# Optimization experiments

Hardware: AMD Instinct MI355X
Metric: run time of the kernel (lower is better)

Reference implementation:

```python
import jax, jax.numpy as jnp
import numpy as np

N_NODES = 100000
N_EDGES = 1_600_000
D_EMB = 64
D_HID = 128


def setup_inputs() -> dict:
    key = jax.random.key(0)
    k1, k2, k3, k4 = jax.random.split(key, 4)
    emb = jax.random.normal(k1, (N_NODES, D_EMB), dtype=jnp.float32)
    W1 = jax.random.normal(k2, (D_EMB, D_HID), dtype=jnp.float32) * 0.05
    b1 = jnp.zeros((D_HID,), dtype=jnp.float32)
    W2 = jax.random.normal(k3, (D_HID, D_EMB), dtype=jnp.float32) * 0.05
    b2 = jnp.zeros((D_EMB,), dtype=jnp.float32)
    edge_index = jax.random.randint(k4, (2, N_EDGES), 0, N_NODES, dtype=jnp.int64 if jax.config.jax_enable_x64 else jnp.int32)
    return {"emb": emb, "W1": W1, "b1": b1, "W2": W2, "b2": b2,
            "edge_index": edge_index, "num_nodes": N_NODES}


def _gcn_conv(x, W, b, src, dst, deg_inv_sqrt, num_nodes):
    # PyG GCNConv: linear transform, then normalized scatter-add aggregation.
    x = x @ W                                   # [N, out]
    norm = deg_inv_sqrt[src] * deg_inv_sqrt[dst]  # [E+N]
    msg = x[src] * norm[:, None]                # gather + scale
    out = jax.ops.segment_sum(msg, dst, num_segments=num_nodes)
    return out + b


def reference(emb, W1, b1, W2, b2, edge_index, num_nodes):
    # Add self-loops (PyG GCNConv default add_self_loops=True).
    loops = jnp.arange(num_nodes, dtype=edge_index.dtype)
    src = jnp.concatenate([edge_index[0], loops])
    dst = jnp.concatenate([edge_index[1], loops])
    # Symmetric normalization degree (computed on destination, incl. loops).
    deg = jax.ops.segment_sum(jnp.ones(src.shape, dtype=emb.dtype), dst,
                              num_segments=num_nodes)
    dinv = jnp.where(deg > 0, jax.lax.rsqrt(jnp.maximum(deg, 1e-12)), 0.0)

    x = _gcn_conv(emb, W1, b1, src, dst, dinv, num_nodes)
    x = jax.nn.relu(x)
    x = _gcn_conv(x, W2, b2, src, dst, dinv, num_nodes)
    return x
```

## Files before the change

### kernel.cpp

```cpp
#include <hip/hip_runtime.h>


constexpr int D_EMB = 64;
constexpr int D_HID = 128;
constexpr int CB_LOG = 9;
constexpr int CB = 1 << CB_LOG;
constexpr int CAP = 16384;
constexpr int FB_EPT = 16;
constexpr int FB_CHUNK = 256 * FB_EPT;

__global__ __launch_bounds__(256) void k_binit(int* __restrict__ bcur) {
    bcur[threadIdx.x * 16] = threadIdx.x * CAP;
}

__global__ __launch_bounds__(256) void k_fillb(const int* __restrict__ ei,
                                               int* __restrict__ bcur,
                                               unsigned int* __restrict__ recs, int E) {
    __shared__ int hist[4][256];
    __shared__ int lcur[256];
    const int tid  = threadIdx.x;
    const int w    = tid >> 6;
    const int base = blockIdx.x * FB_CHUNK;

    for (int i = tid; i < 4 * 256; i += 256) ((int*)hist)[i] = 0;
    __syncthreads();

    int s[FB_EPT], d[FB_EPT];
#pragma unroll
    for (int i = 0; i < FB_EPT; ++i) {
        int e = base + tid + i * 256;
        if (e < E) {
            s[i] = ei[e];
            d[i] = ei[E + e];
            atomicAdd(&hist[w][d[i] >> CB_LOG], 1);
        } else {
            d[i] = -1;
        }
    }
    __syncthreads();

    int h = hist[0][tid] + hist[1][tid] + hist[2][tid] + hist[3][tid];
    if (h > 0) lcur[tid] = atomicAdd(&bcur[tid * 16], h);
    __syncthreads();

#pragma unroll
    for (int i = 0; i < FB_EPT; ++i) {
        if (d[i] >= 0) {
            int b   = d[i] >> CB_LOG;
            int pos = atomicAdd(&lcur[b], 1);
            recs[pos] = ((unsigned int)(d[i] & (CB - 1)) << 23) | (unsigned int)s[i];
        }
    }
}

__global__ __launch_bounds__(256) void k_bscan(const int* __restrict__ bcur,
                                               int* __restrict__ bbase,
                                               int* __restrict__ row_ptr,
                                               int nbuckc, int N, int E) {
    __shared__ int ts[256];
    const int tid = threadIdx.x;
    int s = (tid < nbuckc) ? (bcur[tid * 16] - tid * CAP) : 0;
    ts[tid] = s;
    __syncthreads();
    for (int off = 1; off < 256; off <<= 1) {
        int t = (tid >= off) ? ts[tid - off] : 0;
        __syncthreads();
        ts[tid] += t;
        __syncthreads();
    }
    if (tid < nbuckc) bbase[tid] = ts[tid] - s;
    if (tid == nbuckc - 1) bbase[nbuckc] = ts[tid];
    if (tid == 0) row_ptr[N] = E;
}

__global__ __launch_bounds__(1024) void k_binsort(const unsigned int* __restrict__ recs,
                                                  const int* __restrict__ bbase,
                                                  int* __restrict__ row_ptr,
                                                  float* __restrict__ dinv,
                                                  unsigned int* __restrict__ srcs, int N) {
    __shared__ int ld[CB];
    const int b   = blockIdx.x;
    const int n0  = b * CB;
    const int tid = threadIdx.x;
    const int nn  = min(CB, N - n0);
    const int obeg = bbase[b];
    const int sz   = bbase[b + 1] - obeg;
    const unsigned int* rb = recs + (size_t)b * CAP;

    if (tid < nn) ld[tid] = 0;
    __syncthreads();

    for (int i = tid; i < sz; i += 1024)
        atomicAdd(&ld[rb[i] >> 23], 1);
    __syncthreads();

    int own = (tid < nn) ? ld[tid] : 0;
    for (int off = 1; off < CB; off <<= 1) {
        int t = (tid >= off && tid < nn) ? ld[tid - off] : 0;
        __syncthreads();
        if (tid < nn) ld[tid] += t;
        __syncthreads();
    }
    int incl = (tid < nn) ? ld[tid] : 0;
    __syncthreads();
    if (tid < nn) {
        int rp = obeg + incl - own;
        row_ptr[n0 + tid] = rp;
        dinv[n0 + tid] = rsqrtf((float)(own + 1));
        ld[tid] = rp;
    }
    __syncthreads();

    for (int i = tid; i < sz; i += 1024) {
        unsigned int rec = rb[i];
        int pos = atomicAdd(&ld[rec >> 23], 1);
        srcs[pos] = rec & 0x7FFFFF;
    }
}

template <int K, int OUT, int BM, bool BIAS, bool RELU>
__global__ __launch_bounds__(256) void k_gemm(
    const float* __restrict__ A, const float* __restrict__ W,
    const float* __restrict__ bias, float* __restrict__ X, int N) {
    constexpr int NCG = OUT / 4;
    constexpr int NRG = 256 / NCG;
    constexpr int RPT = BM / NRG;

    __shared__ float As[BM][K + 1];
    __shared__ float Ws[K][OUT];

    const int tid  = threadIdx.x;
    const int row0 = blockIdx.x * BM;

    for (int i = tid; i < K * OUT / 4; i += 256)
        ((float4*)Ws)[i] = ((const float4*)W)[i];

    for (int i = tid; i < BM * K / 4; i += 256) {
        int r  = i / (K / 4);
        int k4 = i % (K / 4);
        int row = row0 + r;
        float4 v = make_float4(0.f, 0.f, 0.f, 0.f);
        if (row < N) v = ((const float4*)(A + (size_t)row * K))[k4];
        As[r][k4 * 4 + 0] = v.x;
        As[r][k4 * 4 + 1] = v.y;
        As[r][k4 * 4 + 2] = v.z;
        As[r][k4 * 4 + 3] = v.w;
    }
    __syncthreads();

    const int tc = tid % NCG;
    const int tr = tid / NCG;
    const int r0 = tr * RPT;

    float acc[RPT][4];
#pragma unroll
    for (int i = 0; i < RPT; ++i)
        acc[i][0] = acc[i][1] = acc[i][2] = acc[i][3] = 0.f;

#pragma unroll 8
    for (int k = 0; k < K; ++k) {
        float4 w = *(const float4*)&Ws[k][tc * 4];
#pragma unroll
        for (int i = 0; i < RPT; ++i) {
            float a = As[r0 + i][k];
            acc[i][0] = fmaf(a, w.x, acc[i][0]);
            acc[i][1] = fmaf(a, w.y, acc[i][1]);
            acc[i][2] = fmaf(a, w.z, acc[i][2]);
            acc[i][3] = fmaf(a, w.w, acc[i][3]);
        }
    }

    float4 bb = make_float4(0.f, 0.f, 0.f, 0.f);
    if (BIAS) bb = ((const float4*)bias)[tc];

#pragma unroll
    for (int i = 0; i < RPT; ++i) {
        int row = row0 + r0 + i;
        if (row >= N) break;
        float4 v = make_float4(acc[i][0], acc[i][1], acc[i][2], acc[i][3]);
        if (BIAS) { v.x += bb.x; v.y += bb.y; v.z += bb.z; v.w += bb.w; }
        if (RELU) {
            v.x = fmaxf(v.x, 0.f); v.y = fmaxf(v.y, 0.f);
            v.z = fmaxf(v.z, 0.f); v.w = fmaxf(v.w, 0.f);
        }
        ((float4*)(X + (size_t)row * OUT))[tc] = v;
    }
}

template <bool BIAS>
__global__ __launch_bounds__(256) void k_gather64(
    const int* __restrict__ row_ptr, const unsigned int* __restrict__ srcs,
    const float* __restrict__ dinv, const float* __restrict__ X,
    const float* __restrict__ bias, float* __restrict__ OUT, int N) {
    const int wid  = (blockIdx.x * 256 + threadIdx.x) >> 6;
    const int lane = threadIdx.x & 63;
    const int q    = lane >> 4;
    const int l    = lane & 15;
    if (wid >= N) return;
    const int v = wid;
    const float dv = dinv[v];
    const int beg = row_ptr[v];
    const int end = row_ptr[v + 1];

    float4 a0 = make_float4(0.f, 0.f, 0.f, 0.f);
    float4 a1 = make_float4(0.f, 0.f, 0.f, 0.f);
    float4 a2 = make_float4(0.f, 0.f, 0.f, 0.f);
    float4 a3 = make_float4(0.f, 0.f, 0.f, 0.f);

    int j0 = beg + q, j1 = j0 + 4, j2 = j0 + 8, j3 = j0 + 12;
    int s0 = (j0 < end) ? (int)srcs[j0] : -1;
    int s1 = (j1 < end) ? (int)srcs[j1] : -1;
    int s2 = (j2 < end) ? (int)srcs[j2] : -1;
    int s3 = (j3 < end) ? (int)srcs[j3] : -1;

    while (j3 < end) {
        const int t0 = s0, t1 = s1, t2 = s2, t3 = s3;
        j0 += 16; j1 += 16; j2 += 16; j3 += 16;
        s0 = (j0 < end) ? (int)srcs[j0] : -1;
        s1 = (j1 < end) ? (int)srcs[j1] : -1;
        s2 = (j2 < end) ? (int)srcs[j2] : -1;
        s3 = (j3 < end) ? (int)srcs[j3] : -1;
        float w0 = dinv[t0] * dv, w1 = dinv[t1] * dv;
        float w2 = dinv[t2] * dv, w3 = dinv[t3] * dv;
        float4 x0 = ((const float4*)(X + (size_t)t0 * 64))[l];
        float4 x1 = ((const float4*)(X + (size_t)t1 * 64))[l];
        float4 x2 = ((const float4*)(X + (size_t)t2 * 64))[l];
        float4 x3 = ((const float4*)(X + (size_t)t3 * 64))[l];
        a0.x = fmaf(x0.x, w0, a0.x); a0.y = fmaf(x0.y, w0, a0.y);
        a0.z = fmaf(x0.z, w0, a0.z); a0.w = fmaf(x0.w, w0, a0.w);
        a1.x = fmaf(x1.x, w1, a1.x); a1.y = fmaf(x1.y, w1, a1.y);
        a1.z = fmaf(x1.z, w1, a1.z); a1.w = fmaf(x1.w, w1, a1.w);
        a2.x = fmaf(x2.x, w2, a2.x); a2.y = fmaf(x2.y, w2, a2.y);
        a2.z = fmaf(x2.z, w2, a2.z); a2.w = fmaf(x2.w, w2, a2.w);
        a3.x = fmaf(x3.x, w3, a3.x); a3.y = fmaf(x3.y, w3, a3.y);
        a3.z = fmaf(x3.z, w3, a3.z); a3.w = fmaf(x3.w, w3, a3.w);
    }
    if (s0 >= 0) {
        float w = dinv[s0] * dv;
        float4 x = ((const float4*)(X + (size_t)s0 * 64))[l];
        a0.x = fmaf(x.x, w, a0.x); a0.y = fmaf(x.y, w, a0.y);
        a0.z = fmaf(x.z, w, a0.z); a0.w = fmaf(x.w, w, a0.w);
    }
    if (s1 >= 0) {
        float w = dinv[s1] * dv;
        float4 x = ((const float4*)(X + (size_t)s1 * 64))[l];
        a1.x = fmaf(x.x, w, a1.x); a1.y = fmaf(x.y, w, a1.y);
        a1.z = fmaf(x.z, w, a1.z); a1.w = fmaf(x.w, w, a1.w);
    }
    if (s2 >= 0) {
        float w = dinv[s2] * dv;
        float4 x = ((const float4*)(X + (size_t)s2 * 64))[l];
        a2.x = fmaf(x.x, w, a2.x); a2.y = fmaf(x.y, w, a2.y);
        a2.z = fmaf(x.z, w, a2.z); a2.w = fmaf(x.w, w, a2.w);
    }
    if (s3 >= 0) {
        float w = dinv[s3] * dv;
        float4 x = ((const float4*)(X + (size_t)s3 * 64))[l];
        a3.x = fmaf(x.x, w, a3.x); a3.y = fmaf(x.y, w, a3.y);
        a3.z = fmaf(x.z, w, a3.z); a3.w = fmaf(x.w, w, a3.w);
    }

    float4 acc = make_float4((a0.x + a1.x) + (a2.x + a3.x),
                             (a0.y + a1.y) + (a2.y + a3.y),
                             (a0.z + a1.z) + (a2.z + a3.z),
                             (a0.w + a1.w) + (a2.w + a3.w));

#pragma unroll
    for (int m = 16; m <= 32; m <<= 1) {
        acc.x += __shfl_xor(acc.x, m);
        acc.y += __shfl_xor(acc.y, m);
        acc.z += __shfl_xor(acc.z, m);
        acc.w += __shfl_xor(acc.w, m);
    }

    if (q == 0) {
        float4 xv = ((const float4*)(X + (size_t)v * 64))[l];
        float s = dv * dv;
        acc.x = fmaf(xv.x, s, acc.x);
        acc.y = fmaf(xv.y, s, acc.y);
        acc.z = fmaf(xv.z, s, acc.z);
        acc.w = fmaf(xv.w, s, acc.w);
        if (BIAS) {
            float4 bb = ((const float4*)bias)[l];
            acc.x += bb.x; acc.y += bb.y; acc.z += bb.z; acc.w += bb.w;
        }
        ((float4*)(OUT + (size_t)v * 64))[l] = acc;
    }
}

extern "C" void kernel_launch(void* const* d_in, const int* in_sizes, int n_in,
                              void* d_out, int out_size, void* d_ws, size_t ws_size,
                              hipStream_t stream) {
    const float* emb = (const float*)d_in[0];
    const float* W1  = (const float*)d_in[1];
    const float* b1  = (const float*)d_in[2];
    const float* W2  = (const float*)d_in[3];
    const float* b2  = (const float*)d_in[4];
    const int*   ei  = (const int*)d_in[5];

    const int N = in_sizes[0] / D_EMB;
    const int E = in_sizes[5] / 2;
    const int nbuckc = (N + CB - 1) / CB;

    float*        a1      = (float*)d_ws;
    float*        h1      = a1 + (size_t)N * D_EMB;
    unsigned int* srcs    = (unsigned int*)(h1 + (size_t)N * D_HID);
    unsigned int* recs    = srcs + E;
    int*          row_ptr = (int*)(recs + (size_t)nbuckc * CAP);
    int*          bcur    = row_ptr + (N + 1);
    int*          bbase   = bcur + 256 * 16;
    float*        dinv    = (float*)(bbase + 257);
    float*        x2      = a1;
    float*        out     = (float*)d_out;

    const int nbFb  = (E + FB_CHUNK - 1) / FB_CHUNK;
    const int nbGat = (N * 64 + 255) / 256;

    k_binit<<<1, 256, 0, stream>>>(bcur);
    k_fillb<<<nbFb, 256, 0, stream>>>(ei, bcur, recs, E);
    k_bscan<<<1, 256, 0, stream>>>(bcur, bbase, row_ptr, nbuckc, N, E);
    k_binsort<<<nbuckc, 1024, 0, stream>>>(recs, bbase, row_ptr, dinv, srcs, N);

    k_gather64<false><<<nbGat, 256, 0, stream>>>(row_ptr, srcs, dinv, emb, nullptr, a1, N);
    k_gemm<D_EMB, D_HID, 64, true, true><<<(N + 63) / 64, 256, 0, stream>>>(a1, W1, b1, h1, N);

    k_gemm<D_HID, D_EMB, 32, false, false><<<(N + 31) / 32, 256, 0, stream>>>(h1, W2, nullptr, x2, N);
    k_gather64<true><<<nbGat, 256, 0, stream>>>(row_ptr, srcs, dinv, x2, b2, out, N);
}
```

Baseline: 312.2 us.

## Store gathered feature tables in bf16 to halve gather traffic

Converts the input embeddings to bf16 in a new pre-pass kernel. The second GEMM now writes its output as packed bf16. Both aggregation passes gather 128-byte bf16 rows with 8 edges in flight per wave instead of 256-byte fp32 rows, accumulating in fp32. This aims to cut the random-gather memory traffic that dominates the aggregation, at the cost of an extra conversion pass and lower input precision that may affect accuracy tolerance.

```diff
diff --git a/kernel.cpp b/kernel.cpp
--- a/kernel.cpp
+++ b/kernel.cpp
@@ -8,6 +8,29 @@
 constexpr int CAP = 16384;
 constexpr int FB_EPT = 16;
 constexpr int FB_CHUNK = 256 * FB_EPT;
+
+__device__ inline unsigned int f2bf1(float f) {
+    unsigned int u = __float_as_uint(f);
+    return (u + 0x7FFFu + ((u >> 16) & 1u)) >> 16;
+}
+__device__ inline float blo(unsigned int u) { return __uint_as_float(u << 16); }
+__device__ inline float bhi(unsigned int u) { return __uint_as_float(u & 0xFFFF0000u); }
+
+__global__ __launch_bounds__(256) void k_f2bf(const float* __restrict__ in,
+                                              uint4* __restrict__ out, int n8) {
+    int i = blockIdx.x * 256 + threadIdx.x;
+    int stride = gridDim.x * 256;
+    for (; i < n8; i += stride) {
+        float4 a = ((const float4*)in)[i * 2];
+        float4 b = ((const float4*)in)[i * 2 + 1];
+        uint4 o;
+        o.x = f2bf1(a.x) | (f2bf1(a.y) << 16);
+        o.y = f2bf1(a.z) | (f2bf1(a.w) << 16);
+        o.z = f2bf1(b.x) | (f2bf1(b.y) << 16);
+        o.w = f2bf1(b.z) | (f2bf1(b.w) << 16);
+        out[i] = o;
+    }
+}
 
 __global__ __launch_bounds__(256) void k_binit(int* __restrict__ bcur) {
     bcur[threadIdx.x * 16] = threadIdx.x * CAP;
@@ -118,10 +141,10 @@
     }
 }
 
-template <int K, int OUT, int BM, bool BIAS, bool RELU>
+template <int K, int OUT, int BM, bool BIAS, bool RELU, bool OUTBF>
 __global__ __launch_bounds__(256) void k_gemm(
     const float* __restrict__ A, const float* __restrict__ W,
-    const float* __restrict__ bias, float* __restrict__ X, int N) {
+    const float* __restrict__ bias, void* __restrict__ Xout, int N) {
     constexpr int NCG = OUT / 4;
     constexpr int NRG = 256 / NCG;
     constexpr int RPT = BM / NRG;
@@ -183,108 +206,73 @@
             v.x = fmaxf(v.x, 0.f); v.y = fmaxf(v.y, 0.f);
             v.z = fmaxf(v.z, 0.f); v.w = fmaxf(v.w, 0.f);
         }
-        ((float4*)(X + (size_t)row * OUT))[tc] = v;
+        if (OUTBF) {
+            unsigned int* Xb = (unsigned int*)Xout;
+            uint2 p;
+            p.x = f2bf1(v.x) | (f2bf1(v.y) << 16);
+            p.y = f2bf1(v.z) | (f2bf1(v.w) << 16);
+            ((uint2*)(Xb + (size_t)row * (OUT / 2)))[tc] = p;
+        } else {
+            ((float4*)((float*)Xout + (size_t)row * OUT))[tc] = v;
+        }
     }
 }
 
 template <bool BIAS>
-__global__ __launch_bounds__(256) void k_gather64(
+__global__ __launch_bounds__(256) void k_gather64b(
     const int* __restrict__ row_ptr, const unsigned int* __restrict__ srcs,
-    const float* __restrict__ dinv, const float* __restrict__ X,
+    const float* __restrict__ dinv, const unsigned int* __restrict__ Xb,
     const float* __restrict__ bias, float* __restrict__ OUT, int N) {
     const int wid  = (blockIdx.x * 256 + threadIdx.x) >> 6;
     const int lane = threadIdx.x & 63;
-    const int q    = lane >> 4;
-    const int l    = lane & 15;
+    const int g    = lane >> 3;
+    const int l    = lane & 7;
     if (wid >= N) return;
     const int v = wid;
     const float dv = dinv[v];
     const int beg = row_ptr[v];
     const int end = row_ptr[v + 1];
 
-    float4 a0 = make_float4(0.f, 0.f, 0.f, 0.f);
-    float4 a1 = make_float4(0.f, 0.f, 0.f, 0.f);
-    float4 a2 = make_float4(0.f, 0.f, 0.f, 0.f);
-    float4 a3 = make_float4(0.f, 0.f, 0.f, 0.f);
-
-    int j0 = beg + q, j1 = j0 + 4, j2 = j0 + 8, j3 = j0 + 12;
-    int s0 = (j0 < end) ? (int)srcs[j0] : -1;
-    int s1 = (j1 < end) ? (int)srcs[j1] : -1;
-    int s2 = (j2 < end) ? (int)srcs[j2] : -1;
-    int s3 = (j3 < end) ? (int)srcs[j3] : -1;
-
-    while (j3 < end) {
-        const int t0 = s0, t1 = s1, t2 = s2, t3 = s3;
-        j0 += 16; j1 += 16; j2 += 16; j3 += 16;
-        s0 = (j0 < end) ? (int)srcs[j0] : -1;
-        s1 = (j1 < end) ? (int)srcs[j1] : -1;
-        s2 = (j2 < end) ? (int)srcs[j2] : -1;
-        s3 = (j3 < end) ? (int)srcs[j3] : -1;
-        float w0 = dinv[t0] * dv, w1 = dinv[t1] * dv;
-        float w2 = dinv[t2] * dv, w3 = dinv[t3] * dv;
-        float4 x0 = ((const float4*)(X + (size_t)t0 * 64))[l];
-        float4 x1 = ((const float4*)(X + (size_t)t1 * 64))[l];
-        float4 x2 = ((const float4*)(X + (size_t)t2 * 64))[l];
-        float4 x3 = ((const float4*)(X + (size_t)t3 * 64))[l];
-        a0.x = fmaf(x0.x, w0, a0.x); a0.y = fmaf(x0.y, w0, a0.y);
-        a0.z = fmaf(x0.z, w0, a0.z); a0.w = fmaf(x0.w, w0, a0.w);
-        a1.x = fmaf(x1.x, w1, a1.x); a1.y = fmaf(x1.y, w1, a1.y);
-        a1.z = fmaf(x1.z, w1, a1.z); a1.w = fmaf(x1.w, w1, a1.w);
-        a2.x = fmaf(x2.x, w2, a2.x); a2.y = fmaf(x2.y, w2, a2.y);
-        a2.z = fmaf(x2.z, w2, a2.z); a2.w = fmaf(x2.w, w2, a2.w);
-        a3.x = fmaf(x3.x, w3, a3.x); a3.y = fmaf(x3.y, w3, a3.y);
-        a3.z = fmaf(x3.z, w3, a3.z); a3.w = fmaf(x3.w, w3, a3.w);
-    }
-    if (s0 >= 0) {
-        float w = dinv[s0] * dv;
-        float4 x = ((const float4*)(X + (size_t)s0 * 64))[l];
-        a0.x = fmaf(x.x, w, a0.x); a0.y = fmaf(x.y, w, a0.y);
-        a0.z = fmaf(x.z, w, a0.z); a0.w = fmaf(x.w, w, a0.w);
-    }
-    if (s1 >= 0) {
-        float w = dinv[s1] * dv;
-        float4 x = ((const float4*)(X + (size_t)s1 * 64))[l];
-        a1.x = fmaf(x.x, w, a1.x); a1.y = fmaf(x.y, w, a1.y);
-        a1.z = fmaf(x.z, w, a1.z); a1.w = fmaf(x.w, w, a1.w);
-    }
-    if (s2 >= 0) {
-        float w = dinv[s2] * dv;
-        float4 x = ((const float4*)(X + (size_t)s2 * 64))[l];
-        a2.x = fmaf(x.x, w, a2.x); a2.y = fmaf(x.y, w, a2.y);
-        a2.z = fmaf(x.z, w, a2.z); a2.w = fmaf(x.w, w, a2.w);
-    }
-    if (s3 >= 0) {
-        float w = dinv[s3] * dv;
-        float4 x = ((const float4*)(X + (size_t)s3 * 64))[l];
-        a3.x = fmaf(x.x, w, a3.x); a3.y = fmaf(x.y, w, a3.y);
-        a3.z = fmaf(x.z, w, a3.z); a3.w = fmaf(x.w, w, a3.w);
-    }
-
-    float4 acc = make_float4((a0.x + a1.x) + (a2.x + a3.x),
-                             (a0.y + a1.y) + (a2.y + a3.y),
-                             (a0.z + a1.z) + (a2.z + a3.z),
-                             (a0.w + a1.w) + (a2.w + a3.w));
-
-#pragma unroll
-    for (int m = 16; m <= 32; m <<= 1) {
-        acc.x += __shfl_xor(acc.x, m);
-        acc.y += __shfl_xor(acc.y, m);
-        acc.z += __shfl_xor(acc.z, m);
-        acc.w += __shfl_xor(acc.w, m);
-    }
-
-    if (q == 0) {
-        float4 xv = ((const float4*)(X + (size_t)v * 64))[l];
-        float s = dv * dv;
-        acc.x = fmaf(xv.x, s, acc.x);
-        acc.y = fmaf(xv.y, s, acc.y);
-        acc.z = fmaf(xv.z, s, acc.z);
-        acc.w = fmaf(xv.w, s, acc.w);
+    float acc[8];
+#pragma unroll
+    for (int i = 0; i < 8; ++i) acc[i] = 0.f;
+
+    int j = beg + g;
+    int s = (j < end) ? (int)srcs[j] : -1;
+    while (s >= 0) {
+        int jn = j + 8;
+        int sn = (jn < end) ? (int)srcs[jn] : -1;
+        float w = dinv[s] * dv;
+        uint4 xb = ((const uint4*)(Xb + (size_t)s * 32))[l];
+        acc[0] = fmaf(blo(xb.x), w, acc[0]); acc[1] = fmaf(bhi(xb.x), w, acc[1]);
+        acc[2] = fmaf(blo(xb.y), w, acc[2]); acc[3] = fmaf(bhi(xb.y), w, acc[3]);
+        acc[4] = fmaf(blo(xb.z), w, acc[4]); acc[5] = fmaf(bhi(xb.z), w, acc[5]);
+        acc[6] = fmaf(blo(xb.w), w, acc[6]); acc[7] = fmaf(bhi(xb.w), w, acc[7]);
+        s = sn; j = jn;
+    }
+
+#pragma unroll
+    for (int m = 8; m <= 32; m <<= 1) {
+#pragma unroll
+        for (int i = 0; i < 8; ++i) acc[i] += __shfl_xor(acc[i], m);
+    }
+
+    if (g == 0) {
+        uint4 xb = ((const uint4*)(Xb + (size_t)v * 32))[l];
+        float s2 = dv * dv;
+        acc[0] = fmaf(blo(xb.x), s2, acc[0]); acc[1] = fmaf(bhi(xb.x), s2, acc[1]);
+        acc[2] = fmaf(blo(xb.y), s2, acc[2]); acc[3] = fmaf(bhi(xb.y), s2, acc[3]);
+        acc[4] = fmaf(blo(xb.z), s2, acc[4]); acc[5] = fmaf(bhi(xb.z), s2, acc[5]);
+        acc[6] = fmaf(blo(xb.w), s2, acc[6]); acc[7] = fmaf(bhi(xb.w), s2, acc[7]);
         if (BIAS) {
-            float4 bb = ((const float4*)bias)[l];
-            acc.x += bb.x; acc.y += bb.y; acc.z += bb.z; acc.w += bb.w;
-        }
-        ((float4*)(OUT + (size_t)v * 64))[l] = acc;
+            float4 b0 = ((const float4*)bias)[l * 2];
+            float4 b1 = ((const float4*)bias)[l * 2 + 1];
+            acc[0] += b0.x; acc[1] += b0.y; acc[2] += b0.z; acc[3] += b0.w;
+            acc[4] += b1.x; acc[5] += b1.y; acc[6] += b1.z; acc[7] += b1.w;
+        }
+        float* orow = OUT + (size_t)v * 64;
+        ((float4*)orow)[l * 2]     = make_float4(acc[0], acc[1], acc[2], acc[3]);
+        ((float4*)orow)[l * 2 + 1] = make_float4(acc[4], acc[5], acc[6], acc[7]);
     }
 }
 
@@ -310,20 +298,23 @@
     int*          bcur    = row_ptr + (N + 1);
     int*          bbase   = bcur + 256 * 16;
     float*        dinv    = (float*)(bbase + 257);
-    float*        x2      = a1;
+    unsigned int* embb    = (unsigned int*)(dinv + N);
+    unsigned int* x2b     = (unsigned int*)a1;
     float*        out     = (float*)d_out;
 
     const int nbFb  = (E + FB_CHUNK - 1) / FB_CHUNK;
     const int nbGat = (N * 64 + 255) / 256;
+
+    k_f2bf<<<2048, 256, 0, stream>>>(emb, (uint4*)embb, N * D_EMB / 8);
 
     k_binit<<<1, 256, 0, stream>>>(bcur);
     k_fillb<<<nbFb, 256, 0, stream>>>(ei, bcur, recs, E);
     k_bscan<<<1, 256, 0, stream>>>(bcur, bbase, row_ptr, nbuckc, N, E);
     k_binsort<<<nbuckc, 1024, 0, stream>>>(recs, bbase, row_ptr, dinv, srcs, N);
 
-    k_gather64<false><<<nbGat, 256, 0, stream>>>(row_ptr, srcs, dinv, emb, nullptr, a1, N);
-    k_gemm<D_EMB, D_HID, 64, true, true><<<(N + 63) / 64, 256, 0, stream>>>(a1, W1, b1, h1, N);
-
-    k_gemm<D_HID, D_EMB, 32, false, false><<<(N + 31) / 32, 256, 0, stream>>>(h1, W2, nullptr, x2, N);
-    k_gather64<true><<<nbGat, 256, 0, stream>>>(row_ptr, srcs, dinv, x2, b2, out, N);
-}
+    k_gather64b<false><<<nbGat, 256, 0, stream>>>(row_ptr, srcs, dinv, embb, nullptr, a1, N);
+    k_gemm<D_EMB, D_HID, 64, true, true, false><<<(N + 63) / 64, 256, 0, stream>>>(a1, W1, b1, h1, N);
+
+    k_gemm<D_HID, D_EMB, 32, false, false, true><<<(N + 31) / 32, 256, 0, stream>>>(h1, W2, nullptr, x2b, N);
+    k_gather64b<true><<<nbGat, 256, 0, stream>>>(row_ptr, srcs, dinv, x2b, b2, out, N);
+}
```

New measurement: 291.9 us. -6.5%, faster.
